# Optimization experiments

Measured on AMD Instinct MI355X. Metric: run time of the kernel, lower is better.

## Reference

```python
import jax, jax.numpy as jnp
import numpy as np

H = 8
D_MODEL = 1024
DIM_G = 64
WAVE_LEN = 1000.0


def box_relational_embedding(f_g):
    # f_g: [B, N, 4] -> [B, N, N, 64] trigonometric geometry embedding
    B, N, _ = f_g.shape
    x_min, y_min, x_max, y_max = jnp.split(f_g, 4, axis=-1)  # each [B, N, 1]
    cx = (x_min + x_max) * 0.5
    cy = (y_min + y_max) * 0.5
    w = x_max - x_min + 1.0
    h = y_max - y_min + 1.0
    # row i vs column j deltas, normalized by row box size
    dx = jnp.log(jnp.maximum(jnp.abs((cx - cx.reshape(B, 1, N)) / w), 1e-3))
    dy = jnp.log(jnp.maximum(jnp.abs((cy - cy.reshape(B, 1, N)) / h), 1e-3))
    dw = jnp.log(w / w.reshape(B, 1, N))
    dh = jnp.log(h / h.reshape(B, 1, N))
    pos = jnp.stack([dx, dy, dw, dh], axis=-1)  # [B, N, N, 4]
    feat_range = jnp.arange(DIM_G // 8, dtype=jnp.float32) / (DIM_G / 8.0)
    dim_mat = 1.0 / jnp.power(WAVE_LEN, feat_range)  # [8]
    mul = (100.0 * pos)[..., None] * dim_mat  # [B, N, N, 4, 8]
    mul = mul.reshape(B, N, N, DIM_G // 2)
    return jnp.concatenate([jnp.sin(mul), jnp.cos(mul)], axis=-1)  # [B, N, N, 64]


def setup_inputs() -> dict:
    key = jax.random.key(0)
    ks = jax.random.split(key, 12)
    B, N, D = 16, 256, D_MODEL
    q = jax.random.normal(ks[0], (B, N, D), jnp.float32)
    k = jax.random.normal(ks[1], (B, N, D), jnp.float32)
    v = jax.random.normal(ks[2], (B, N, D), jnp.float32)
    # valid boxes: x_max > x_min, y_max > y_min
    xy = jax.random.uniform(ks[3], (B, N, 2), jnp.float32) * 100.0
    wh = jax.random.uniform(ks[4], (B, N, 2), jnp.float32) * 50.0 + 1.0
    input_box = jnp.concatenate([xy, xy + wh], axis=-1)  # [B, N, 4]
    s = 0.02
    Wq = jax.random.normal(ks[5], (D, D), jnp.float32) * s
    Wk = jax.random.normal(ks[6], (D, D), jnp.float32) * s
    Wv = jax.random.normal(ks[7], (D, D), jnp.float32) * s
    Wo = jax.random.normal(ks[8], (D, D), jnp.float32) * s
    bq = jnp.zeros((D,), jnp.float32)
    bk = jnp.zeros((D,), jnp.float32)
    bv = jnp.zeros((D,), jnp.float32)
    bo = jnp.zeros((D,), jnp.float32)
    Wg = jax.random.normal(ks[9], (H, DIM_G), jnp.float32) * 0.1  # stacked per-head Linear(64,1)
    bg = jax.random.normal(ks[10], (H,), jnp.float32) * 0.1
    return {"input_query": q, "input_key": k, "input_value": v, "input_box": input_box,
            "Wq": Wq, "bq": bq, "Wk": Wk, "bk": bk, "Wv": Wv, "bv": bv,
            "Wg": Wg, "bg": bg, "Wo": Wo, "bo": bo}


def reference(input_query, input_key, input_value, input_box,
              Wq, bq, Wk, bk, Wv, bv, Wg, bg, Wo, bo):
    B, N, D = input_query.shape
    d_k = D // H

    def proj(x, W, b):
        return (x @ W + b).reshape(B, N, H, d_k).transpose(0, 2, 1, 3)  # [B,H,N,dk]

    q = proj(input_query, Wq, bq)
    k = proj(input_key, Wk, bk)
    v = proj(input_value, Wv, bv)

    emb = box_relational_embedding(input_box)  # [B, N, N, 64]
    # per-head Linear(64 -> 1), stacked: [B, H, N, N]
    rel_w = jax.nn.relu(jnp.einsum('bmng,hg->bhmn', emb, Wg) + bg[None, :, None, None])

    scores = jnp.einsum('bhqd,bhkd->bhqk', q, k) / np.sqrt(d_k).astype(np.float32)
    logits = jnp.log(jnp.maximum(rel_w, 1e-6)) + scores
    attn = jax.nn.softmax(logits, axis=-1)  # [B, H, N, N]
    out = jnp.einsum('bhqk,bhkd->bhqd', attn, v)
    out = out.transpose(0, 2, 1, 3).reshape(B, N, D)
    return out @ Wo + bo
```

## Files before the change

kernel.cpp:

```cpp
#include <hip/hip_runtime.h>
#include <hip/hip_bf16.h>
#include <hip/hip_fp16.h>
#include <math.h>

#define B_  16
#define N_  256
#define D_  1024
#define H_  8
#define DK_ 128

typedef unsigned short u16;
typedef __attribute__((ext_vector_type(8))) short s8v;
typedef __attribute__((ext_vector_type(4))) float f4v;

__device__ __forceinline__ u16 f2b(float x) {
    union { float f; unsigned u; } v; v.f = x;
    unsigned r = v.u + 0x7fffu + ((v.u >> 16) & 1u);
    return (u16)(r >> 16);
}

__device__ __forceinline__ void gload16(void* lds, const void* g) {
    __builtin_amdgcn_global_load_lds(
        (const __attribute__((address_space(1))) void*)g,
        (__attribute__((address_space(3))) void*)lds, 16, 0, 0);
}

__device__ __forceinline__ void waitv8() { asm volatile("s_waitcnt vmcnt(8)" ::: "memory"); }
__device__ __forceinline__ void waitv6() { asm volatile("s_waitcnt vmcnt(6)" ::: "memory"); }
__device__ __forceinline__ void waitv4() { asm volatile("s_waitcnt vmcnt(4)" ::: "memory"); }
__device__ __forceinline__ void waitv3() { asm volatile("s_waitcnt vmcnt(3)" ::: "memory"); }
__device__ __forceinline__ void waitv0() { asm volatile("s_waitcnt vmcnt(0)" ::: "memory"); }
__device__ __forceinline__ void membar() { asm volatile("" ::: "memory"); }

__global__ __launch_bounds__(256)
void prep_kernel(const float* __restrict__ x0, const float* __restrict__ x1,
                 const float* __restrict__ x2,
                 const float* __restrict__ W0, const float* __restrict__ W1,
                 const float* __restrict__ W2, const float* __restrict__ W3,
                 u16* __restrict__ xb, u16* __restrict__ Wt)
{
    const int bx = blockIdx.x;
    const int tid = threadIdx.x;
    if (bx < 6144) {
        const int y = bx >> 11;
        const float* in = (y == 0) ? x0 : (y == 1) ? x1 : x2;
        u16* o = xb + (size_t)y * 4194304;
        const int i = (bx & 2047) * 256 + tid;
        const float4 a = ((const float4*)in)[2 * i];
        const float4 b = ((const float4*)in)[2 * i + 1];
        union { u16 s[8]; uint4 v; } t;
        t.s[0] = f2b(a.x); t.s[1] = f2b(a.y); t.s[2] = f2b(a.z); t.s[3] = f2b(a.w);
        t.s[4] = f2b(b.x); t.s[5] = f2b(b.y); t.s[6] = f2b(b.z); t.s[7] = f2b(b.w);
        ((uint4*)o)[i] = t.v;
    } else {
        __shared__ float t[32][33];
        const int tt = bx - 6144;
        const int z  = tt >> 10;
        const int rem = tt & 1023;
        const int k0 = (rem & 31) * 32;
        const int n0 = (rem >> 5) * 32;
        const float* W = (z == 0) ? W0 : (z == 1) ? W1 : (z == 2) ? W2 : W3;
        u16* o = Wt + (size_t)z * (D_ * D_);
        const int c = tid & 31, r8 = tid >> 5;
#pragma unroll
        for (int rr = 0; rr < 4; ++rr)
            t[r8 + rr * 8][c] = W[(size_t)(k0 + r8 + rr * 8) * D_ + n0 + c];
        __syncthreads();
#pragma unroll
        for (int rr = 0; rr < 4; ++rr)
            o[(size_t)(n0 + r8 + rr * 8) * D_ + k0 + c] = f2b(t[c][r8 + rr * 8]);
    }
}

template<int BM, int FM, int LOADS, int MODE>
__global__ __launch_bounds__(256)
void gemm_kernel(const u16* __restrict__ A0, const u16* __restrict__ Wt0,
                 const float* __restrict__ b0, const float* __restrict__ b1,
                 const float* __restrict__ b2, void* __restrict__ outb)
{
    constexpr int WM  = FM * 16;
    constexpr int MT8 = (4096 / BM) / 8;
    __shared__ __align__(16) u16 As[3][BM][32];
    __shared__ __align__(16) u16 Bs[3][128][32];

    const int z = blockIdx.z;
    const u16* A  = A0  + (size_t)z * 4194304;
    const u16* Wt = Wt0 + (size_t)z * 1048576;
    const float* bias = (z == 0) ? b0 : (z == 1) ? b1 : b2;

    const int bid = blockIdx.x;
    const int xcd = bid & 7;
    const int wic = bid >> 3;
    const int by  = xcd * MT8 + (wic & (MT8 - 1));
    const int bx  = wic / MT8;
    const int m0  = by * BM;
    const int n0  = bx * 128;

    const int tid  = threadIdx.x;
    const int lane = tid & 63;
    const int w    = tid >> 6;
    const int l15  = lane & 15;
    const int l4   = lane >> 4;
    const int wr   = w >> 1;
    const int wc   = w & 1;

    const int gr   = tid >> 2;
    const int c4   = tid & 3;
    const int scol = (c4 ^ ((gr >> 1) & 3)) * 8;
    const int doff = c4 * 8;
    const u16* asrc = A  + (size_t)(m0 + gr) * 1024 + scol;
    const u16* bsrc = Wt + (size_t)(n0 + gr) * 1024 + scol;
    const int fc = (l4 ^ ((l15 >> 1) & 3)) * 8;

    auto stage = [&](int buf, int kt) {
        const int k0_ = kt * 32;
        gload16(&As[buf][gr][doff], asrc + k0_);
        if constexpr (BM == 128)
            gload16(&As[buf][gr + 64][doff], asrc + 64 * 1024 + k0_);
        gload16(&Bs[buf][gr][doff], bsrc + k0_);
        gload16(&Bs[buf][gr + 64][doff], bsrc + 64 * 1024 + k0_);
    };

    f4v acc[FM][4] = {};

    stage(0, 0);
    stage(1, 1);
    int cur = 0, stg = 2;

    for (int kt = 0; kt < 32; ++kt) {
        membar();
        __builtin_amdgcn_s_barrier();
        if (kt < 30) {
            stage(stg, kt + 2);
            if constexpr (LOADS == 4) waitv8(); else waitv6();
        } else if (kt == 30) {
            if constexpr (LOADS == 4) waitv4(); else waitv3();
        } else {
            waitv0();
        }
        membar();
        __builtin_amdgcn_s_barrier();

        s8v af[FM], bf[4];
#pragma unroll
        for (int i = 0; i < FM; ++i)
            af[i] = *(const s8v*)&As[cur][wr * WM + i * 16 + l15][fc];
#pragma unroll
        for (int j = 0; j < 4; ++j)
            bf[j] = *(const s8v*)&Bs[cur][wc * 64 + j * 16 + l15][fc];
#pragma unroll
        for (int i = 0; i < FM; ++i)
#pragma unroll
            for (int j = 0; j < 4; ++j)
                acc[i][j] = __builtin_amdgcn_mfma_f32_16x16x32_bf16(
                    af[i], bf[j], acc[i][j], 0, 0, 0);

        cur = (cur == 2) ? 0 : cur + 1;
        stg = (stg == 2) ? 0 : stg + 1;
    }

#pragma unroll
    for (int j = 0; j < 4; ++j) {
        const int n = n0 + wc * 64 + j * 16 + l15;
        const float bb = bias[n];
#pragma unroll
        for (int i = 0; i < FM; ++i) {
            const int mbase = m0 + wr * WM + i * 16 + l4 * 4;
            if constexpr (MODE == 0) {
#pragma unroll
                for (int reg = 0; reg < 4; ++reg)
                    ((float*)outb)[(size_t)(mbase + reg) * 1024 + n] =
                        acc[i][j][reg] + bb;
            } else {
                if (z == 2) {
                    const int b = mbase >> 8, tok = mbase & 255;
                    const int h = n >> 7, d = n & 127;
                    ushort4 st;
                    st.x = f2b(acc[i][j][0] + bb);
                    st.y = f2b(acc[i][j][1] + bb);
                    st.z = f2b(acc[i][j][2] + bb);
                    st.w = f2b(acc[i][j][3] + bb);
                    *(ushort4*)&((u16*)outb)[(size_t)z * 4194304 +
                        (((size_t)b * H_ + h) * DK_ + d) * N_ + tok] = st;
                } else {
                    const int h = n >> 7, d = n & 127;
#pragma unroll
                    for (int reg = 0; reg < 4; ++reg) {
                        const int m = mbase + reg;
                        const int b = m >> 8, tok = m & 255;
                        ((u16*)outb)[(size_t)z * 4194304 +
                            (((size_t)b * H_ + h) * N_ + tok) * DK_ + d] =
                            f2b(acc[i][j][reg] + bb);
                    }
                }
            }
        }
    }
}

__global__ __launch_bounds__(256)
void boxbias_kernel(const float* __restrict__ fg, const float* __restrict__ Wg,
                    const float* __restrict__ bg, _Float16* __restrict__ lb)
{
    const int tid = threadIdx.x;
    const int b = blockIdx.x >> 8;
    const int i = blockIdx.x & 255;

    const float4 bi = *(const float4*)&fg[(size_t)(b * N_ + i) * 4];
    const float cxi = 0.5f * (bi.x + bi.z);
    const float cyi = 0.5f * (bi.y + bi.w);
    const float wi  = bi.z - bi.x + 1.0f;
    const float hi  = bi.w - bi.y + 1.0f;

    const int j = tid;
    const float4 bj = *(const float4*)&fg[(size_t)(b * N_ + j) * 4];
    const float cxj = 0.5f * (bj.x + bj.z);
    const float cyj = 0.5f * (bj.y + bj.w);
    const float wj  = bj.z - bj.x + 1.0f;
    const float hj  = bj.w - bj.y + 1.0f;

    const float pos[4] = {
        logf(fmaxf(fabsf((cxi - cxj) / wi), 1e-3f)) * 100.0f,
        logf(fmaxf(fabsf((cyi - cyj) / hi), 1e-3f)) * 100.0f,
        logf(wi / wj) * 100.0f,
        logf(hi / hj) * 100.0f
    };
    const float dim[8] = {1.0f, 0.421696503f, 0.177827941f, 0.0749894209f,
                          0.0316227766f, 0.0133352143f, 0.00562341325f, 0.00237137371f};

    float sv[32], cv[32];
#pragma unroll
    for (int p = 0; p < 4; ++p)
#pragma unroll
        for (int q = 0; q < 8; ++q)
            __sincosf(pos[p] * dim[q], &sv[p * 8 + q], &cv[p * 8 + q]);

#pragma unroll
    for (int h = 0; h < 8; ++h) {
        float acc = bg[h];
        const float* wrow = Wg + h * 64;
#pragma unroll
        for (int g = 0; g < 32; ++g)
            acc = fmaf(sv[g], wrow[g], fmaf(cv[g], wrow[32 + g], acc));
        const float rel = fmaxf(acc, 0.0f);
        lb[(((size_t)b * H_ + h) * N_ + i) * N_ + j] =
            (_Float16)logf(fmaxf(rel, 1e-6f));
    }
}

__global__ __launch_bounds__(256)
void attn_mfma_kernel(const u16* __restrict__ qp, const u16* __restrict__ kp,
                      const u16* __restrict__ vp, const _Float16* __restrict__ lb,
                      u16* __restrict__ ao)
{
    __shared__ __align__(16) u16 Ks[32][136];
    __shared__ __align__(16) u16 Vt[128][40];
    __shared__ __align__(16) u16 Ps[4][16][40];

    const int tid  = threadIdx.x;
    const int lane = tid & 63;
    const int w    = tid >> 6;
    const int l15  = lane & 15;
    const int l4   = lane >> 4;
    const int bh   = blockIdx.x >> 2;
    const int qt   = blockIdx.x & 3;
    const int q0   = qt * 64 + w * 16;

    s8v qf[4];
    const u16* qb = qp + ((size_t)bh * N_ + q0) * DK_;
#pragma unroll
    for (int ks = 0; ks < 4; ++ks)
        qf[ks] = *(const s8v*)(qb + (size_t)l15 * DK_ + ks * 32 + l4 * 8);

    f4v o[8] = {};
    float m_r[4], l_r[4];
#pragma unroll
    for (int r = 0; r < 4; ++r) { m_r[r] = -INFINITY; l_r[r] = 0.0f; }

    const float scale = 0.08838834764831845f;
    const _Float16* lbb = lb + ((size_t)bh * N_ + q0) * N_;

    const int sr = tid >> 3;
    const int sc = (tid & 7) * 16;
    const int vr = tid >> 2;
    const int vs = (tid & 3) * 8;

    for (int kt = 0; kt < 8; ++kt) {
        __syncthreads();
        {
            const u16* ksrc = kp + ((size_t)bh * N_ + kt * 32) * DK_;
            *(s8v*)&Ks[sr][sc]     = *(const s8v*)(ksrc + (size_t)sr * DK_ + sc);
            *(s8v*)&Ks[sr][sc + 8] = *(const s8v*)(ksrc + (size_t)sr * DK_ + sc + 8);
        }
        {
            const u16* vsrc = vp + ((size_t)bh * DK_ + vr) * N_ + kt * 32 + vs;
            const s8v v0 = *(const s8v*)vsrc;
            const s8v v1 = *(const s8v*)(vsrc + 64 * N_);
            *(s8v*)&Vt[vr][vs]      = v0;
            *(s8v*)&Vt[vr + 64][vs] = v1;
        }
        __syncthreads();

        f4v s[2] = {};
#pragma unroll
        for (int ks = 0; ks < 4; ++ks) {
#pragma unroll
            for (int kf = 0; kf < 2; ++kf) {
                const s8v kb = *(const s8v*)&Ks[kf * 16 + l15][ks * 32 + l4 * 8];
                s[kf] = __builtin_amdgcn_mfma_f32_16x16x32_bf16(
                    qf[ks], kb, s[kf], 0, 0, 0);
            }
        }
#pragma unroll
        for (int kf = 0; kf < 2; ++kf)
#pragma unroll
            for (int r = 0; r < 4; ++r)
                s[kf][r] = fmaf(s[kf][r], scale, (float)
                    lbb[(size_t)(l4 * 4 + r) * N_ + kt * 32 + kf * 16 + l15]);

        {
            float rm[4], al[4];
#pragma unroll
            for (int r = 0; r < 4; ++r) rm[r] = fmaxf(s[0][r], s[1][r]);
#pragma unroll
            for (int st = 1; st <= 8; st <<= 1)
#pragma unroll
                for (int r = 0; r < 4; ++r) rm[r] = fmaxf(rm[r], __shfl_xor(rm[r], st));
#pragma unroll
            for (int r = 0; r < 4; ++r) {
                const float mn = fmaxf(m_r[r], rm[r]);
                al[r] = __expf(m_r[r] - mn);
                m_r[r] = mn;
            }
            float p0[4], p1[4], rs[4];
#pragma unroll
            for (int r = 0; r < 4; ++r) {
                p0[r] = __expf(s[0][r] - m_r[r]);
                p1[r] = __expf(s[1][r] - m_r[r]);
                rs[r] = p0[r] + p1[r];
            }
#pragma unroll
            for (int st = 1; st <= 8; st <<= 1)
#pragma unroll
                for (int r = 0; r < 4; ++r) rs[r] += __shfl_xor(rs[r], st);
#pragma unroll
            for (int r = 0; r < 4; ++r) {
                l_r[r] = l_r[r] * al[r] + rs[r];
                Ps[w][l4 * 4 + r][l15]      = f2b(p0[r]);
                Ps[w][l4 * 4 + r][16 + l15] = f2b(p1[r]);
            }
#pragma unroll
            for (int nf = 0; nf < 8; ++nf)
#pragma unroll
                for (int r = 0; r < 4; ++r) o[nf][r] *= al[r];
        }

        const s8v pa = *(const s8v*)&Ps[w][l15][l4 * 8];
#pragma unroll
        for (int nf = 0; nf < 8; ++nf) {
            const s8v vb = *(const s8v*)&Vt[nf * 16 + l15][l4 * 8];
            o[nf] = __builtin_amdgcn_mfma_f32_16x16x32_bf16(pa, vb, o[nf], 0, 0, 0);
        }
    }

    const int b = bh >> 3, h = bh & 7;
    float inv[4];
#pragma unroll
    for (int r = 0; r < 4; ++r) inv[r] = 1.0f / l_r[r];
#pragma unroll
    for (int nf = 0; nf < 8; ++nf) {
#pragma unroll
        for (int r = 0; r < 4; ++r) {
            const int tok = q0 + l4 * 4 + r;
            const int d = nf * 16 + l15;
            ao[(((size_t)b * N_ + tok) * H_ + h) * DK_ + d] = f2b(o[nf][r] * inv[r]);
        }
    }
}

extern "C" void kernel_launch(void* const* d_in, const int* in_sizes, int n_in,
                              void* d_out, int out_size, void* d_ws, size_t ws_size,
                              hipStream_t stream)
{
    const float* xq = (const float*)d_in[0];
    const float* xk = (const float*)d_in[1];
    const float* xv = (const float*)d_in[2];
    const float* fg = (const float*)d_in[3];
    const float* Wq = (const float*)d_in[4];
    const float* bq = (const float*)d_in[5];
    const float* Wk = (const float*)d_in[6];
    const float* bk = (const float*)d_in[7];
    const float* Wv = (const float*)d_in[8];
    const float* bv = (const float*)d_in[9];
    const float* Wg = (const float*)d_in[10];
    const float* bg = (const float*)d_in[11];
    const float* Wo = (const float*)d_in[12];
    const float* bo = (const float*)d_in[13];

    char* w8 = (char*)d_ws;
    u16*      xb  = (u16*)(w8);
    u16*      Wt  = (u16*)(w8 + 25165824);
    u16*      qkv = (u16*)(w8 + 33554432);
    _Float16* lb  = (_Float16*)(w8 + 58720256);
    u16*      ao  = (u16*)(w8 + 75497472);

    prep_kernel<<<10240, 256, 0, stream>>>(xq, xk, xv, Wq, Wk, Wv, Wo, xb, Wt);

    gemm_kernel<128, 4, 4, 1><<<dim3(256, 1, 3), 256, 0, stream>>>(
        xb, Wt, bq, bk, bv, qkv);

    boxbias_kernel<<<B_ * N_, 256, 0, stream>>>(fg, Wg, bg, lb);

    attn_mfma_kernel<<<512, 256, 0, stream>>>(
        qkv, qkv + 4194304, qkv + 2 * 4194304, lb, ao);

    gemm_kernel<64, 2, 3, 0><<<dim3(512, 1, 1), 256, 0, stream>>>(
        ao, Wt + 3 * 1048576, bo, bo, bo, d_out);
}
```

Baseline: 124.7 us.

## Fuse box-bias into prep kernel and double-buffer K/V tiles in attention

```diff
diff --git a/kernel.cpp b/kernel.cpp
--- a/kernel.cpp
+++ b/kernel.cpp
@@ -37,7 +37,9 @@
                  const float* __restrict__ x2,
                  const float* __restrict__ W0, const float* __restrict__ W1,
                  const float* __restrict__ W2, const float* __restrict__ W3,
-                 u16* __restrict__ xb, u16* __restrict__ Wt)
+                 u16* __restrict__ xb, u16* __restrict__ Wt,
+                 const float* __restrict__ fg, const float* __restrict__ Wg,
+                 const float* __restrict__ bg, _Float16* __restrict__ lb)
 {
     const int bx = blockIdx.x;
     const int tid = threadIdx.x;
@@ -52,7 +54,7 @@
         t.s[0] = f2b(a.x); t.s[1] = f2b(a.y); t.s[2] = f2b(a.z); t.s[3] = f2b(a.w);
         t.s[4] = f2b(b.x); t.s[5] = f2b(b.y); t.s[6] = f2b(b.z); t.s[7] = f2b(b.w);
         ((uint4*)o)[i] = t.v;
-    } else {
+    } else if (bx < 10240) {
         __shared__ float t[32][33];
         const int tt = bx - 6144;
         const int z  = tt >> 10;
@@ -69,6 +71,51 @@
 #pragma unroll
         for (int rr = 0; rr < 4; ++rr)
             o[(size_t)(n0 + r8 + rr * 8) * D_ + k0 + c] = f2b(t[c][r8 + rr * 8]);
+    } else {
+        const int bb = bx - 10240;
+        const int b = bb >> 8;
+        const int i = bb & 255;
+
+        const float4 bi = *(const float4*)&fg[(size_t)(b * N_ + i) * 4];
+        const float cxi = 0.5f * (bi.x + bi.z);
+        const float cyi = 0.5f * (bi.y + bi.w);
+        const float wi  = bi.z - bi.x + 1.0f;
+        const float hi  = bi.w - bi.y + 1.0f;
+
+        const int j = tid;
+        const float4 bj = *(const float4*)&fg[(size_t)(b * N_ + j) * 4];
+        const float cxj = 0.5f * (bj.x + bj.z);
+        const float cyj = 0.5f * (bj.y + bj.w);
+        const float wj  = bj.z - bj.x + 1.0f;
+        const float hj  = bj.w - bj.y + 1.0f;
+
+        const float pos[4] = {
+            logf(fmaxf(fabsf((cxi - cxj) / wi), 1e-3f)) * 100.0f,
+            logf(fmaxf(fabsf((cyi - cyj) / hi), 1e-3f)) * 100.0f,
+            logf(wi / wj) * 100.0f,
+            logf(hi / hj) * 100.0f
+        };
+        const float dim[8] = {1.0f, 0.421696503f, 0.177827941f, 0.0749894209f,
+                              0.0316227766f, 0.0133352143f, 0.00562341325f, 0.00237137371f};
+
+        float sv[32], cv[32];
+#pragma unroll
+        for (int p = 0; p < 4; ++p)
+#pragma unroll
+            for (int q = 0; q < 8; ++q)
+                __sincosf(pos[p] * dim[q], &sv[p * 8 + q], &cv[p * 8 + q]);
+
+#pragma unroll
+        for (int h = 0; h < 8; ++h) {
+            float acc = bg[h];
+            const float* wrow = Wg + h * 64;
+#pragma unroll
+            for (int g = 0; g < 32; ++g)
+                acc = fmaf(sv[g], wrow[g], fmaf(cv[g], wrow[32 + g], acc));
+            const float rel = fmaxf(acc, 0.0f);
+            lb[(((size_t)b * H_ + h) * N_ + i) * N_ + j] =
+                (_Float16)logf(fmaxf(rel, 1e-6f));
+        }
     }
 }
 
@@ -199,62 +246,12 @@
 }
 
 __global__ __launch_bounds__(256)
-void boxbias_kernel(const float* __restrict__ fg, const float* __restrict__ Wg,
-                    const float* __restrict__ bg, _Float16* __restrict__ lb)
-{
-    const int tid = threadIdx.x;
-    const int b = blockIdx.x >> 8;
-    const int i = blockIdx.x & 255;
-
-    const float4 bi = *(const float4*)&fg[(size_t)(b * N_ + i) * 4];
-    const float cxi = 0.5f * (bi.x + bi.z);
-    const float cyi = 0.5f * (bi.y + bi.w);
-    const float wi  = bi.z - bi.x + 1.0f;
-    const float hi  = bi.w - bi.y + 1.0f;
-
-    const int j = tid;
-    const float4 bj = *(const float4*)&fg[(size_t)(b * N_ + j) * 4];
-    const float cxj = 0.5f * (bj.x + bj.z);
-    const float cyj = 0.5f * (bj.y + bj.w);
-    const float wj  = bj.z - bj.x + 1.0f;
-    const float hj  = bj.w - bj.y + 1.0f;
-
-    const float pos[4] = {
-        logf(fmaxf(fabsf((cxi - cxj) / wi), 1e-3f)) * 100.0f,
-        logf(fmaxf(fabsf((cyi - cyj) / hi), 1e-3f)) * 100.0f,
-        logf(wi / wj) * 100.0f,
-        logf(hi / hj) * 100.0f
-    };
-    const float dim[8] = {1.0f, 0.421696503f, 0.177827941f, 0.0749894209f,
-                          0.0316227766f, 0.0133352143f, 0.00562341325f, 0.00237137371f};
-
-    float sv[32], cv[32];
-#pragma unroll
-    for (int p = 0; p < 4; ++p)
-#pragma unroll
-        for (int q = 0; q < 8; ++q)
-            __sincosf(pos[p] * dim[q], &sv[p * 8 + q], &cv[p * 8 + q]);
-
-#pragma unroll
-    for (int h = 0; h < 8; ++h) {
-        float acc = bg[h];
-        const float* wrow = Wg + h * 64;
-#pragma unroll
-        for (int g = 0; g < 32; ++g)
-            acc = fmaf(sv[g], wrow[g], fmaf(cv[g], wrow[32 + g], acc));
-        const float rel = fmaxf(acc, 0.0f);
-        lb[(((size_t)b * H_ + h) * N_ + i) * N_ + j] =
-            (_Float16)logf(fmaxf(rel, 1e-6f));
-    }
-}
-
-__global__ __launch_bounds__(256)
 void attn_mfma_kernel(const u16* __restrict__ qp, const u16* __restrict__ kp,
                       const u16* __restrict__ vp, const _Float16* __restrict__ lb,
                       u16* __restrict__ ao)
 {
-    __shared__ __align__(16) u16 Ks[32][136];
-    __shared__ __align__(16) u16 Vt[128][40];
+    __shared__ __align__(16) u16 Ks[2][32][136];
+    __shared__ __align__(16) u16 Vt[2][128][40];
     __shared__ __align__(16) u16 Ps[4][16][40];
 
     const int tid  = threadIdx.x;
@@ -285,28 +282,37 @@
     const int vr = tid >> 2;
     const int vs = (tid & 3) * 8;
 
+    const u16* kbase = kp + (size_t)bh * N_ * DK_ + (size_t)sr * DK_ + sc;
+    const u16* vbase = vp + ((size_t)bh * DK_ + vr) * N_ + vs;
+
+    s8v kr0, kr1, vv0, vv1;
+    auto ldtile = [&](int kt) {
+        kr0 = *(const s8v*)(kbase + (size_t)kt * 32 * DK_);
+        kr1 = *(const s8v*)(kbase + (size_t)kt * 32 * DK_ + 8);
+        vv0 = *(const s8v*)(vbase + kt * 32);
+        vv1 = *(const s8v*)(vbase + 64 * N_ + kt * 32);
+    };
+    auto wrtile = [&](int buf) {
+        *(s8v*)&Ks[buf][sr][sc]     = kr0;
+        *(s8v*)&Ks[buf][sr][sc + 8] = kr1;
+        *(s8v*)&Vt[buf][vr][vs]      = vv0;
+        *(s8v*)&Vt[buf][vr + 64][vs] = vv1;
+    };
+
+    ldtile(0);
+    wrtile(0);
+
+    int cur = 0;
     for (int kt = 0; kt < 8; ++kt) {
+        if (kt < 7) ldtile(kt + 1);
         __syncthreads();
-        {
-            const u16* ksrc = kp + ((size_t)bh * N_ + kt * 32) * DK_;
-            *(s8v*)&Ks[sr][sc]     = *(const s8v*)(ksrc + (size_t)sr * DK_ + sc);
-            *(s8v*)&Ks[sr][sc + 8] = *(const s8v*)(ksrc + (size_t)sr * DK_ + sc + 8);
-        }
-        {
-            const u16* vsrc = vp + ((size_t)bh * DK_ + vr) * N_ + kt * 32 + vs;
-            const s8v v0 = *(const s8v*)vsrc;
-            const s8v v1 = *(const s8v*)(vsrc + 64 * N_);
-            *(s8v*)&Vt[vr][vs]      = v0;
-            *(s8v*)&Vt[vr + 64][vs] = v1;
-        }
-        __syncthreads();
 
         f4v s[2] = {};
 #pragma unroll
         for (int ks = 0; ks < 4; ++ks) {
 #pragma unroll
             for (int kf = 0; kf < 2; ++kf) {
-                const s8v kb = *(const s8v*)&Ks[kf * 16 + l15][ks * 32 + l4 * 8];
+                const s8v kb = *(const s8v*)&Ks[cur][kf * 16 + l15][ks * 32 + l4 * 8];
                 s[kf] = __builtin_amdgcn_mfma_f32_16x16x32_bf16(
                     qf[ks], kb, s[kf], 0, 0, 0);
             }
@@ -358,9 +364,12 @@
         const s8v pa = *(const s8v*)&Ps[w][l15][l4 * 8];
 #pragma unroll
         for (int nf = 0; nf < 8; ++nf) {
-            const s8v vb = *(const s8v*)&Vt[nf * 16 + l15][l4 * 8];
+            const s8v vb = *(const s8v*)&Vt[cur][nf * 16 + l15][l4 * 8];
             o[nf] = __builtin_amdgcn_mfma_f32_16x16x32_bf16(pa, vb, o[nf], 0, 0, 0);
         }
+
+        if (kt < 7) wrtile(cur ^ 1);
+        cur ^= 1;
     }
 
     const int b = bh >> 3, h = bh & 7;
@@ -404,13 +413,12 @@
     _Float16* lb  = (_Float16*)(w8 + 58720256);
     u16*      ao  = (u16*)(w8 + 75497472);
 
-    prep_kernel<<<10240, 256, 0, stream>>>(xq, xk, xv, Wq, Wk, Wv, Wo, xb, Wt);
+    prep_kernel<<<14336, 256, 0, stream>>>(xq, xk, xv, Wq, Wk, Wv, Wo,
+                                           xb, Wt, fg, Wg, bg, lb);
 
     gemm_kernel<128, 4, 4, 1><<<dim3(256, 1, 3), 256, 0, stream>>>(
         xb, Wt, bq, bk, bv, qkv);
 
-    boxbias_kernel<<<B_ * N_, 256, 0, stream>>>(fg, Wg, bg, lb);
-
     attn_mfma_kernel<<<512, 256, 0, stream>>>(
         qkv, qkv + 4194304, qkv + 2 * 4194304, lb, ao);
 
```

After: 129.2 us. 3.7% more time.

## Fuse fp32-to-bf16 activation conversion into QKV projection GEMM loads

Applied to the files above, without the earlier changes.

```diff
diff --git a/kernel.cpp b/kernel.cpp
--- a/kernel.cpp
+++ b/kernel.cpp
@@ -29,46 +29,203 @@
 __device__ __forceinline__ void waitv6() { asm volatile("s_waitcnt vmcnt(6)" ::: "memory"); }
 __device__ __forceinline__ void waitv4() { asm volatile("s_waitcnt vmcnt(4)" ::: "memory"); }
 __device__ __forceinline__ void waitv3() { asm volatile("s_waitcnt vmcnt(3)" ::: "memory"); }
+__device__ __forceinline__ void waitv2() { asm volatile("s_waitcnt vmcnt(2)" ::: "memory"); }
 __device__ __forceinline__ void waitv0() { asm volatile("s_waitcnt vmcnt(0)" ::: "memory"); }
+__device__ __forceinline__ void lgkm0() { asm volatile("s_waitcnt lgkmcnt(0)" ::: "memory"); }
 __device__ __forceinline__ void membar() { asm volatile("" ::: "memory"); }
+#define BAR() __builtin_amdgcn_s_barrier()
 
 __global__ __launch_bounds__(256)
-void prep_kernel(const float* __restrict__ x0, const float* __restrict__ x1,
-                 const float* __restrict__ x2,
-                 const float* __restrict__ W0, const float* __restrict__ W1,
+void prep_kernel(const float* __restrict__ W0, const float* __restrict__ W1,
                  const float* __restrict__ W2, const float* __restrict__ W3,
-                 u16* __restrict__ xb, u16* __restrict__ Wt)
+                 u16* __restrict__ Wt)
 {
-    const int bx = blockIdx.x;
+    __shared__ float t[32][33];
     const int tid = threadIdx.x;
-    if (bx < 6144) {
-        const int y = bx >> 11;
-        const float* in = (y == 0) ? x0 : (y == 1) ? x1 : x2;
-        u16* o = xb + (size_t)y * 4194304;
-        const int i = (bx & 2047) * 256 + tid;
-        const float4 a = ((const float4*)in)[2 * i];
-        const float4 b = ((const float4*)in)[2 * i + 1];
-        union { u16 s[8]; uint4 v; } t;
-        t.s[0] = f2b(a.x); t.s[1] = f2b(a.y); t.s[2] = f2b(a.z); t.s[3] = f2b(a.w);
-        t.s[4] = f2b(b.x); t.s[5] = f2b(b.y); t.s[6] = f2b(b.z); t.s[7] = f2b(b.w);
-        ((uint4*)o)[i] = t.v;
-    } else {
-        __shared__ float t[32][33];
-        const int tt = bx - 6144;
-        const int z  = tt >> 10;
-        const int rem = tt & 1023;
-        const int k0 = (rem & 31) * 32;
-        const int n0 = (rem >> 5) * 32;
-        const float* W = (z == 0) ? W0 : (z == 1) ? W1 : (z == 2) ? W2 : W3;
-        u16* o = Wt + (size_t)z * (D_ * D_);
-        const int c = tid & 31, r8 = tid >> 5;
-#pragma unroll
-        for (int rr = 0; rr < 4; ++rr)
-            t[r8 + rr * 8][c] = W[(size_t)(k0 + r8 + rr * 8) * D_ + n0 + c];
-        __syncthreads();
-#pragma unroll
-        for (int rr = 0; rr < 4; ++rr)
-            o[(size_t)(n0 + r8 + rr * 8) * D_ + k0 + c] = f2b(t[c][r8 + rr * 8]);
+    const int tt = blockIdx.x;
+    const int z  = tt >> 10;
+    const int rem = tt & 1023;
+    const int k0 = (rem & 31) * 32;
+    const int n0 = (rem >> 5) * 32;
+    const float* W = (z == 0) ? W0 : (z == 1) ? W1 : (z == 2) ? W2 : W3;
+    u16* o = Wt + (size_t)z * (D_ * D_);
+    const int c = tid & 31, r8 = tid >> 5;
+#pragma unroll
+    for (int rr = 0; rr < 4; ++rr)
+        t[r8 + rr * 8][c] = W[(size_t)(k0 + r8 + rr * 8) * D_ + n0 + c];
+    __syncthreads();
+#pragma unroll
+    for (int rr = 0; rr < 4; ++rr)
+        o[(size_t)(n0 + r8 + rr * 8) * D_ + k0 + c] = f2b(t[c][r8 + rr * 8]);
+}
+
+__global__ __launch_bounds__(256)
+void qkv_f32a_kernel(const float* __restrict__ xq, const float* __restrict__ xk,
+                     const float* __restrict__ xv, const u16* __restrict__ Wt0,
+                     const float* __restrict__ b0, const float* __restrict__ b1,
+                     const float* __restrict__ b2, u16* __restrict__ qkv)
+{
+    __shared__ __align__(16) u16 As[3][128][32];
+    __shared__ __align__(16) u16 Bs[3][128][32];
+
+    const int z = blockIdx.z;
+    const float* X = (z == 0) ? xq : (z == 1) ? xk : xv;
+    const u16* Wt = Wt0 + (size_t)z * 1048576;
+    const float* bias = (z == 0) ? b0 : (z == 1) ? b1 : b2;
+
+    const int bid = blockIdx.x;
+    const int xcd = bid & 7;
+    const int wic = bid >> 3;
+    const int by  = xcd * 4 + (wic & 3);
+    const int bx  = wic >> 2;
+    const int m0  = by * 128;
+    const int n0  = bx * 128;
+
+    const int tid  = threadIdx.x;
+    const int lane = tid & 63;
+    const int w    = tid >> 6;
+    const int l15  = lane & 15;
+    const int l4   = lane >> 4;
+    const int wr   = w >> 1;
+    const int wc   = w & 1;
+
+    const int gr   = tid >> 2;
+    const int c4   = tid & 3;
+    const int scol = (c4 ^ ((gr >> 1) & 3)) * 8;
+    const int doff = c4 * 8;
+    const u16* bsrc = Wt + (size_t)(n0 + gr) * 1024 + scol;
+
+    const int tr = tid >> 1;
+    const int tc = (tid & 1) * 16;
+    const float* xsrc = X + (size_t)(m0 + tr) * 1024 + tc;
+    const int sw = (tr >> 1) & 3;
+    const int c0 = (tid & 1) * 2;
+    const int d0 = (c0 ^ sw) * 8;
+    const int d1 = ((c0 + 1) ^ sw) * 8;
+
+    const int fc = (l4 ^ ((l15 >> 1) & 3)) * 8;
+
+    float4 a0[4], a1[4];
+#define LDA(dst, kt) do { \
+        const float* p_ = xsrc + (kt) * 32; \
+        dst[0] = *(const float4*)(p_);      dst[1] = *(const float4*)(p_ + 4); \
+        dst[2] = *(const float4*)(p_ + 8);  dst[3] = *(const float4*)(p_ + 12); \
+    } while (0)
+#define WRA(buf, src) do { \
+        union { u16 s[8]; uint4 v; } t0_, t1_; \
+        t0_.s[0] = f2b(src[0].x); t0_.s[1] = f2b(src[0].y); \
+        t0_.s[2] = f2b(src[0].z); t0_.s[3] = f2b(src[0].w); \
+        t0_.s[4] = f2b(src[1].x); t0_.s[5] = f2b(src[1].y); \
+        t0_.s[6] = f2b(src[1].z); t0_.s[7] = f2b(src[1].w); \
+        t1_.s[0] = f2b(src[2].x); t1_.s[1] = f2b(src[2].y); \
+        t1_.s[2] = f2b(src[2].z); t1_.s[3] = f2b(src[2].w); \
+        t1_.s[4] = f2b(src[3].x); t1_.s[5] = f2b(src[3].y); \
+        t1_.s[6] = f2b(src[3].z); t1_.s[7] = f2b(src[3].w); \
+        *(uint4*)&As[buf][tr][d0] = t0_.v; \
+        *(uint4*)&As[buf][tr][d1] = t1_.v; \
+    } while (0)
+#define STGB(buf, kt) do { \
+        const int k0_ = (kt) * 32; \
+        gload16(&Bs[buf][gr][doff],      bsrc + k0_); \
+        gload16(&Bs[buf][gr + 64][doff], bsrc + 64 * 1024 + k0_); \
+    } while (0)
+
+    f4v acc[4][4] = {};
+
+    LDA(a0, 0);
+    WRA(0, a0);
+    STGB(0, 0);
+    LDA(a1, 1);
+    STGB(1, 1);
+    lgkm0(); membar();
+    BAR();
+
+    int cur = 0, wb = 1, bstg = 2;
+
+#define COMPUTE() do { \
+        s8v af_[4], bf_[4]; \
+        _Pragma("unroll") \
+        for (int i = 0; i < 4; ++i) \
+            af_[i] = *(const s8v*)&As[cur][wr * 64 + i * 16 + l15][fc]; \
+        _Pragma("unroll") \
+        for (int j = 0; j < 4; ++j) \
+            bf_[j] = *(const s8v*)&Bs[cur][wc * 64 + j * 16 + l15][fc]; \
+        _Pragma("unroll") \
+        for (int i = 0; i < 4; ++i) \
+            _Pragma("unroll") \
+            for (int j = 0; j < 4; ++j) \
+                acc[i][j] = __builtin_amdgcn_mfma_f32_16x16x32_bf16( \
+                    af_[i], bf_[j], acc[i][j], 0, 0, 0); \
+        cur = (cur == 2) ? 0 : cur + 1; \
+        wb  = (wb  == 2) ? 0 : wb  + 1; \
+        bstg = (bstg == 2) ? 0 : bstg + 1; \
+    } while (0)
+
+#pragma unroll 1
+    for (int kt = 0; kt < 30; kt += 2) {
+        membar(); BAR();
+        LDA(a0, kt + 2);
+        STGB(bstg, kt + 2);
+        waitv8();
+        WRA(wb, a1);
+        lgkm0(); membar();
+        BAR();
+        COMPUTE();
+        membar(); BAR();
+        LDA(a1, kt + 3);
+        STGB(bstg, kt + 3);
+        waitv8();
+        WRA(wb, a0);
+        lgkm0(); membar();
+        BAR();
+        COMPUTE();
+    }
+    membar(); BAR();
+    waitv2();
+    WRA(wb, a1);
+    lgkm0(); membar();
+    BAR();
+    COMPUTE();
+    membar(); BAR();
+    waitv0();
+    membar();
+    BAR();
+    COMPUTE();
+
+#undef COMPUTE
+#undef STGB
+#undef WRA
+#undef LDA
+
+#pragma unroll
+    for (int j = 0; j < 4; ++j) {
+        const int n = n0 + wc * 64 + j * 16 + l15;
+        const float bb = bias[n];
+#pragma unroll
+        for (int i = 0; i < 4; ++i) {
+            const int mbase = m0 + wr * 64 + i * 16 + l4 * 4;
+            if (z == 2) {
+                const int b = mbase >> 8, tok = mbase & 255;
+                const int h = n >> 7, d = n & 127;
+                ushort4 st;
+                st.x = f2b(acc[i][j][0] + bb);
+                st.y = f2b(acc[i][j][1] + bb);
+                st.z = f2b(acc[i][j][2] + bb);
+                st.w = f2b(acc[i][j][3] + bb);
+                *(ushort4*)&qkv[(size_t)z * 4194304 +
+                    (((size_t)b * H_ + h) * DK_ + d) * N_ + tok] = st;
+            } else {
+                const int h = n >> 7, d = n & 127;
+#pragma unroll
+                for (int reg = 0; reg < 4; ++reg) {
+                    const int m = mbase + reg;
+                    const int b = m >> 8, tok = m & 255;
+                    qkv[(size_t)z * 4194304 +
+                        (((size_t)b * H_ + h) * N_ + tok) * DK_ + d] =
+                        f2b(acc[i][j][reg] + bb);
+                }
+            }
+        }
     }
 }
 
@@ -197,6 +354,9 @@
         }
     }
 }
+
+template __global__ void gemm_kernel<128, 4, 4, 1>(
+    const u16*, const u16*, const float*, const float*, const float*, void*);
 
 __global__ __launch_bounds__(256)
 void boxbias_kernel(const float* __restrict__ fg, const float* __restrict__ Wg,
@@ -398,16 +558,15 @@
     const float* bo = (const float*)d_in[13];
 
     char* w8 = (char*)d_ws;
-    u16*      xb  = (u16*)(w8);
     u16*      Wt  = (u16*)(w8 + 25165824);
     u16*      qkv = (u16*)(w8 + 33554432);
     _Float16* lb  = (_Float16*)(w8 + 58720256);
     u16*      ao  = (u16*)(w8 + 75497472);
 
-    prep_kernel<<<10240, 256, 0, stream>>>(xq, xk, xv, Wq, Wk, Wv, Wo, xb, Wt);
-
-    gemm_kernel<128, 4, 4, 1><<<dim3(256, 1, 3), 256, 0, stream>>>(
-        xb, Wt, bq, bk, bv, qkv);
+    prep_kernel<<<4096, 256, 0, stream>>>(Wq, Wk, Wv, Wo, Wt);
+
+    qkv_f32a_kernel<<<dim3(256, 1, 3), 256, 0, stream>>>(
+        xq, xk, xv, Wt, bq, bk, bv, qkv);
 
     boxbias_kernel<<<B_ * N_, 256, 0, stream>>>(fg, Wg, bg, lb);
 
```

New measurement: 128.4 us. +3.0%, slower.
